# Kernel optimization log

Hardware: AMD Instinct MI355X
Metric: run time of the kernel (lower is better)

## Reference

```python
import jax, jax.numpy as jnp
import numpy as np

TEMPERATURE = 0.5
EPS = 1e-12  # torch F.normalize eps


def setup_inputs() -> dict:
    key = jax.random.key(0)
    k1, k2 = jax.random.split(key)
    z_i = jax.random.normal(k1, (32, 128, 128), dtype=jnp.float32)
    z_j = jax.random.normal(k2, (32, 128, 128), dtype=jnp.float32)
    return {"z_i": z_i, "z_j": z_j}


def _l2_normalize(x):
    # matches torch F.normalize(dim=1): x / max(||x||, eps)
    n = jnp.sqrt(jnp.sum(x * x, axis=1, keepdims=True))
    return x / jnp.maximum(n, EPS)


def _off_diagonal(a):
    # rows of a with the diagonal removed, row-major order -> [n, n-1]
    n = a.shape[0]
    return a.reshape(-1)[:-1].reshape(n - 1, n + 1)[:, 1:].reshape(n, n - 1)


def reference(z_i, z_j):
    B, S, D = z_i.shape
    N = B * S
    zi = _l2_normalize(z_i.reshape(N, D))
    zj = _l2_normalize(z_j.reshape(N, D))
    r = jnp.concatenate([zi, zj], axis=0)              # [2N, D]
    sim = r @ r.T                                      # [2N, 2N]
    # positives: off-diagonals at +/-N (unaffected by the diag -inf fill)
    pos = jnp.concatenate([jnp.diagonal(sim, N), jnp.diagonal(sim, -N)])  # [2N]
    # negatives: all non-diagonal entries, row-major (== torch boolean-mask view)
    neg = _off_diagonal(sim)                           # [2N, 2N-1]
    logits = jnp.concatenate([pos[:, None], neg], axis=1) / TEMPERATURE  # [2N, 2N]
    # labels are all 0 -> CE(sum) / 2N == mean of -log_softmax[:, 0]
    loss = -jax.nn.log_softmax(logits, axis=1)[:, 0]
    return jnp.sum(loss) / (2 * N)
```

## Files before the change

### kernel.cpp

```cpp
#include <hip/hip_runtime.h>
#include <hip/hip_bf16.h>
#include <math.h>

#define NPAIR 4096
#define D 128
#define TWO_N 8192
#define NSLAB 32
#define ALPHA 1.6986436f

typedef float f32x4 __attribute__((ext_vector_type(4)));
typedef int i32x8 __attribute__((ext_vector_type(8)));

__device__ __forceinline__ void async_ld16(void* lds, const void* g) {
    __builtin_amdgcn_global_load_lds(
        (__attribute__((address_space(1))) const unsigned int*)g,
        (__attribute__((address_space(3))) unsigned int*)lds, 16, 0, 0);
}

__device__ __forceinline__ i32x8 mk8(uint4 lo, uint4 hi) {
    return (i32x8){(int)lo.x, (int)lo.y, (int)lo.z, (int)lo.w,
                   (int)hi.x, (int)hi.y, (int)hi.z, (int)hi.w};
}

__global__ __launch_bounds__(256) void norm_kernel(const float* __restrict__ zi,
                                                   const float* __restrict__ zj,
                                                   unsigned char* __restrict__ Rb,
                                                   float* __restrict__ pos,
                                                   float* __restrict__ out) {
    if (blockIdx.x == 0 && threadIdx.x == 0) out[0] = 0.f;
    int k = blockIdx.x * 4 + (threadIdx.x >> 6);
    int t = threadIdx.x & 63;
    const float2 a = *(const float2*)(zi + k * D + 2 * t);
    const float2 b = *(const float2*)(zj + k * D + 2 * t);
    float si = a.x * a.x + a.y * a.y;
    float sj = b.x * b.x + b.y * b.y;
    float dt = a.x * b.x + a.y * b.y;
    #pragma unroll
    for (int m = 1; m < 64; m <<= 1) {
        si += __shfl_xor(si, m, 64);
        sj += __shfl_xor(sj, m, 64);
        dt += __shfl_xor(dt, m, 64);
    }
    float ii = 1.0f / fmaxf(sqrtf(si), 1e-12f);
    float ij = 1.0f / fmaxf(sqrtf(sj), 1e-12f);
    if (t == 0) pos[k] = dt * ii * ij;
    ii *= ALPHA; ij *= ALPHA;
    int r0 = __builtin_amdgcn_cvt_pk_fp8_f32(a.x * ii, a.y * ii, 0, false);
    *(unsigned short*)(Rb + (size_t)k * 128 + 2 * t) = (unsigned short)r0;
    int r1 = __builtin_amdgcn_cvt_pk_fp8_f32(b.x * ij, b.y * ij, 0, false);
    *(unsigned short*)(Rb + (size_t)(k + NPAIR) * 128 + 2 * t) = (unsigned short)r1;
}

__global__ __launch_bounds__(256, 4) void simexp_kernel(const unsigned char* __restrict__ Rb,
                                                        float* __restrict__ rspart) {
    __shared__ uint4 Bs[4][3][128];
    const int bi = blockIdx.x >> 3;
    const int jc = blockIdx.x & 7;
    const int tid = threadIdx.x;
    const int wave = tid >> 6, lane = tid & 63;
    const int rp = lane & 15, q = lane >> 4;

    i32x8 afr[4];
    {
        const unsigned char* Ab = Rb + (size_t)(bi * 64 + rp) * 128 + q * 32;
        #pragma unroll
        for (int rt = 0; rt < 4; ++rt) {
            uint4 h0 = *(const uint4*)(Ab + rt * 16 * 128);
            uint4 h1 = *(const uint4*)(Ab + rt * 16 * 128 + 16);
            afr[rt] = mk8(h0, h1);
        }
    }

    const unsigned char* gslab = Rb + (size_t)(jc * 1024 + wave * 16) * 128;
    char* lpanel = (char*)&Bs[wave][0][0];
    const int laneoff = (lane >> 3) * 128 + (((lane & 7) ^ ((lane >> 3) & 7)) << 4);

    float rs[16];
    #pragma unroll
    for (int i = 0; i < 16; ++i) rs[i] = 0.f;

    #pragma unroll
    for (int j = 0; j < 2; ++j)
        #pragma unroll
        for (int d = 0; d < 2; ++d)
            async_ld16(lpanel + j * 2048 + d * 1024,
                       gslab + j * 8192 + d * 1024 + laneoff);

    const int diagbase = bi * 64 - jc * 1024;
    const int slot0 = rp * 8;
    const int sw = rp & 7;

    #pragma unroll
    for (int jt = 0; jt < 16; ++jt) {
        if (jt < 14) __builtin_amdgcn_s_waitcnt(0x0F72);
        else         __builtin_amdgcn_s_waitcnt(0x0F70);

        const int cur = jt % 3;
        const uint4* P = &Bs[wave][cur][0];
        uint4 u0 = P[slot0 + ((q * 2 + 0) ^ sw)];
        uint4 u1 = P[slot0 + ((q * 2 + 1) ^ sw)];
        i32x8 bfr = mk8(u0, u1);

        if (jt < 14) {
            const int nb = (jt + 2) % 3;
            #pragma unroll
            for (int d = 0; d < 2; ++d)
                async_ld16(lpanel + nb * 2048 + d * 1024,
                           gslab + (jt + 2) * 8192 + d * 1024 + laneoff);
        }

        f32x4 acc[4] = {};
        #pragma unroll
        for (int rt = 0; rt < 4; ++rt)
            acc[rt] = __builtin_amdgcn_mfma_scale_f32_16x16x128_f8f6f4(
                afr[rt], bfr, acc[rt],
                0, 0,
                0, 0x7F7F7F7F,
                0, 0x7F7F7F7F);

        if (jt * 64 == diagbase) {
            #pragma unroll
            for (int rt = 0; rt < 4; ++rt)
                #pragma unroll
                for (int r = 0; r < 4; ++r) {
                    int ro = rt * 16 + q * 4 + r;
                    int co = wave * 16 + rp;
                    float e = __builtin_amdgcn_exp2f(acc[rt][r]);
                    rs[rt * 4 + r] += (ro == co) ? 0.f : e;
                }
        } else {
            #pragma unroll
            for (int rt = 0; rt < 4; ++rt)
                #pragma unroll
                for (int r = 0; r < 4; ++r)
                    rs[rt * 4 + r] += __builtin_amdgcn_exp2f(acc[rt][r]);
        }
    }

    #pragma unroll
    for (int i = 0; i < 16; ++i) {
        float v = rs[i];
        v += __shfl_xor(v, 1, 64);
        v += __shfl_xor(v, 2, 64);
        v += __shfl_xor(v, 4, 64);
        v += __shfl_xor(v, 8, 64);
        rs[i] = v;
    }
    if (rp == 0) {
        const int slab = jc * 4 + wave;
        const int rowb = bi * 64 + q * 4;
        #pragma unroll
        for (int rt = 0; rt < 4; ++rt)
            #pragma unroll
            for (int r = 0; r < 4; ++r)
                rspart[slab * TWO_N + rowb + rt * 16 + r] = rs[rt * 4 + r];
    }
}

__global__ __launch_bounds__(256) void finalize_kernel(const float* __restrict__ rspart,
                                                       const float* __restrict__ pos,
                                                       float* __restrict__ out) {
    __shared__ float red[4];
    int tid = threadIdx.x;
    float local = 0.f;
    #pragma unroll
    for (int i = 0; i < 2; ++i) {
        int k = blockIdx.x * 512 + i * 256 + tid;
        float rsum = 0.f;
        #pragma unroll
        for (int p = 0; p < NSLAB; ++p) rsum += rspart[p * TWO_N + k];
        float ps = pos[k & (NPAIR - 1)];
        float p2 = ps + ps;
        local += logf(rsum + __expf(p2)) - p2;
    }
    #pragma unroll
    for (int m = 1; m < 64; m <<= 1) local += __shfl_xor(local, m, 64);
    if ((tid & 63) == 0) red[tid >> 6] = local;
    __syncthreads();
    if (tid == 0) {
        float s = red[0] + red[1] + red[2] + red[3];
        atomicAdd(out, s * (1.0f / (float)TWO_N));
    }
}

extern "C" void kernel_launch(void* const* d_in, const int* in_sizes, int n_in,
                              void* d_out, int out_size, void* d_ws, size_t ws_size,
                              hipStream_t stream) {
    const float* zi = (const float*)d_in[0];
    const float* zj = (const float*)d_in[1];
    char* ws = (char*)d_ws;
    unsigned char* Rb = (unsigned char*)ws;
    float* rspart = (float*)(ws + 1 * 1024 * 1024);
    float* pos = (float*)(ws + 2 * 1024 * 1024);

    norm_kernel<<<NPAIR / 4, 256, 0, stream>>>(zi, zj, Rb, pos, (float*)d_out);
    simexp_kernel<<<128 * 8, 256, 0, stream>>>(Rb, rspart);
    finalize_kernel<<<16, 256, 0, stream>>>(rspart, pos, (float*)d_out);
}
```

Baseline: 77.18 us.

## Fuse finalize into simexp via atomic row sums and last-block reduction

Drops the separate finalize kernel. Each simexp block now adds its per-row partial sums into a global rowsum array with atomics, and bumps a per-row-block counter. The last of the 8 blocks for a row block computes the log terms and adds them to the output. This removes one kernel launch and the 32-slab partial buffer pass, at the cost of float atomics and nondeterministic summation order.

```diff
diff --git a/kernel.cpp b/kernel.cpp
--- a/kernel.cpp
+++ b/kernel.cpp
@@ -5,7 +5,6 @@
 #define NPAIR 4096
 #define D 128
 #define TWO_N 8192
-#define NSLAB 32
 #define ALPHA 1.6986436f
 
 typedef float f32x4 __attribute__((ext_vector_type(4)));
@@ -26,8 +25,16 @@
                                                    const float* __restrict__ zj,
                                                    unsigned char* __restrict__ Rb,
                                                    float* __restrict__ pos,
+                                                   float* __restrict__ rowsum,
+                                                   int* __restrict__ cnt,
                                                    float* __restrict__ out) {
-    if (blockIdx.x == 0 && threadIdx.x == 0) out[0] = 0.f;
+    if (threadIdx.x < 8) rowsum[blockIdx.x * 8 + threadIdx.x] = 0.f;
+    if (blockIdx.x == 0) {
+        if (threadIdx.x >= 128 && threadIdx.x < 256) {
+            cnt[threadIdx.x - 128] = 0;
+        }
+        if (threadIdx.x == 8) out[0] = 0.f;
+    }
     int k = blockIdx.x * 4 + (threadIdx.x >> 6);
     int t = threadIdx.x & 63;
     const float2 a = *(const float2*)(zi + k * D + 2 * t);
@@ -52,8 +59,12 @@
 }
 
 __global__ __launch_bounds__(256, 4) void simexp_kernel(const unsigned char* __restrict__ Rb,
-                                                        float* __restrict__ rspart) {
+                                                        float* __restrict__ rowsum,
+                                                        int* __restrict__ cnt,
+                                                        const float* __restrict__ pos,
+                                                        float* __restrict__ out) {
     __shared__ uint4 Bs[4][3][128];
+    __shared__ int oldv;
     const int bi = blockIdx.x >> 3;
     const int jc = blockIdx.x & 7;
     const int tid = threadIdx.x;
@@ -147,39 +158,29 @@
         rs[i] = v;
     }
     if (rp == 0) {
-        const int slab = jc * 4 + wave;
         const int rowb = bi * 64 + q * 4;
         #pragma unroll
         for (int rt = 0; rt < 4; ++rt)
             #pragma unroll
             for (int r = 0; r < 4; ++r)
-                rspart[slab * TWO_N + rowb + rt * 16 + r] = rs[rt * 4 + r];
-    }
-}
-
-__global__ __launch_bounds__(256) void finalize_kernel(const float* __restrict__ rspart,
-                                                       const float* __restrict__ pos,
-                                                       float* __restrict__ out) {
-    __shared__ float red[4];
-    int tid = threadIdx.x;
-    float local = 0.f;
-    #pragma unroll
-    for (int i = 0; i < 2; ++i) {
-        int k = blockIdx.x * 512 + i * 256 + tid;
-        float rsum = 0.f;
-        #pragma unroll
-        for (int p = 0; p < NSLAB; ++p) rsum += rspart[p * TWO_N + k];
-        float ps = pos[k & (NPAIR - 1)];
-        float p2 = ps + ps;
-        local += logf(rsum + __expf(p2)) - p2;
-    }
-    #pragma unroll
-    for (int m = 1; m < 64; m <<= 1) local += __shfl_xor(local, m, 64);
-    if ((tid & 63) == 0) red[tid >> 6] = local;
+                atomicAdd(&rowsum[rowb + rt * 16 + r], rs[rt * 4 + r]);
+    }
+
     __syncthreads();
     if (tid == 0) {
-        float s = red[0] + red[1] + red[2] + red[3];
-        atomicAdd(out, s * (1.0f / (float)TWO_N));
+        __threadfence();
+        oldv = atomicAdd(&cnt[bi], 1);
+    }
+    __syncthreads();
+    if (oldv == 7 && tid < 64) {
+        int rgl = bi * 64 + tid;
+        float rsum = atomicAdd(&rowsum[rgl], 0.0f);
+        float ps = pos[rgl & (NPAIR - 1)];
+        float p2 = ps + ps;
+        float term = __logf(rsum + __expf(p2)) - p2;
+        #pragma unroll
+        for (int m = 1; m < 64; m <<= 1) term += __shfl_xor(term, m, 64);
+        if (tid == 0) atomicAdd(out, term * (1.0f / (float)TWO_N));
     }
 }
 
@@ -190,10 +191,10 @@
     const float* zj = (const float*)d_in[1];
     char* ws = (char*)d_ws;
     unsigned char* Rb = (unsigned char*)ws;
-    float* rspart = (float*)(ws + 1 * 1024 * 1024);
-    float* pos = (float*)(ws + 2 * 1024 * 1024);
-
-    norm_kernel<<<NPAIR / 4, 256, 0, stream>>>(zi, zj, Rb, pos, (float*)d_out);
-    simexp_kernel<<<128 * 8, 256, 0, stream>>>(Rb, rspart);
-    finalize_kernel<<<16, 256, 0, stream>>>(rspart, pos, (float*)d_out);
-}
+    float* rowsum = (float*)(ws + 1024 * 1024);
+    int* cnt = (int*)(ws + 1024 * 1024 + 32 * 1024);
+    float* pos = (float*)(ws + 1024 * 1024 + 64 * 1024);
+
+    norm_kernel<<<NPAIR / 4, 256, 0, stream>>>(zi, zj, Rb, pos, rowsum, cnt, (float*)d_out);
+    simexp_kernel<<<128 * 8, 256, 0, stream>>>(Rb, rowsum, cnt, pos, (float*)d_out);
+}
```

After: 91.66 us. 18.8% more time.
